# Kernel tuning notes

Hardware: AMD Instinct MI355X
Metric: run time of the kernel (lower is better)

Reference implementation:

```python
import jax, jax.numpy as jnp
import numpy as np

# dims: S=batch, P=num_patches, Q=patch_pixels, CB=convolution_bond, R=bond_dim, C=output classes, N=num_carriages
S, P, Q = 512, 196, 48
CB, R, C = 8, 32, 10
N = 8
SC = 0.05  # param init scale to keep the length-8 contraction chain numerically tame


def setup_inputs() -> dict:
    key = jax.random.key(0)
    ks = jax.random.split(key, 7)
    f32 = jnp.float32
    return {
        "x": jax.random.normal(ks[0], (S, P, Q), f32),
        # conv blocks: first has left CB bond squeezed, last has right CB bond squeezed
        "conv_first": jax.random.normal(ks[1], (Q, CB), f32) * SC,
        "conv_mid": jax.random.normal(ks[2], (N - 2, CB, Q, CB), f32) * SC,
        "conv_last": jax.random.normal(ks[3], (CB, Q), f32) * SC,
        # train blocks: first has r_l squeezed and carries the output index c;
        # middle/last have c=1 (squeezed); last has r_r squeezed
        "train_first": jax.random.normal(ks[4], (C, P, R), f32) * SC,
        "train_mid": jax.random.normal(ks[5], (N - 2, R, P, R), f32) * SC,
        "train_last": jax.random.normal(ks[6], (R, P), f32) * SC,
    }


def reference(x, conv_first, conv_mid, conv_last, train_first, train_mid, train_last):
    # Carriage 1: contract X with C1 over patch_pixels, with A1 over patches.
    # state[s, b(CB bond), r(train bond), c(output)]
    state = jnp.einsum('spq,qb,cpr->sbrc', x, conv_first, train_first)

    def step(state, blocks):
        Ck, Ak = blocks  # Ck: [a,q,b], Ak: [l,p,r]
        M = jnp.einsum('spq,aqb->spab', x, Ck)          # [s,p,a,b]
        G = jnp.einsum('spab,lpr->sablr', M, Ak)        # [s,a,b,l,r] per-carriage node
        # contract incoming CB bond (a) and train bond (l) with state
        new_state = jnp.einsum('salc,sablr->sbrc', state, G)
        return new_state, None

    state, _ = jax.lax.scan(step, state, (conv_mid, train_mid))

    # Last carriage: both right bonds squeezed
    GN = jnp.einsum('spq,aq,lp->sal', x, conv_last, train_last)  # [s,a,l]
    out = jnp.einsum('salc,sal->sc', state, GN)  # [S, C]
    return out
```

## Files before the change

### kernel.cpp

```cpp
#include <hip/hip_runtime.h>


typedef _Float16 half8 __attribute__((ext_vector_type(8)));
typedef _Float16 half4 __attribute__((ext_vector_type(4)));
typedef __fp16   fp16x2 __attribute__((ext_vector_type(2)));
typedef float floatx4 __attribute__((ext_vector_type(4)));

#define KP 224
#define LDA2 232
#define GSTR 40
#define SSTR 264

__device__ __forceinline__ void gld_lds16(const void* g, void* l) {
  __builtin_amdgcn_global_load_lds((const __attribute__((address_space(1))) void*)g,
                                   (__attribute__((address_space(3))) void*)l, 16, 0, 0);
}

__global__ __launch_bounds__(256)
void gemm_23(const _Float16* __restrict__ MtF, const _Float16* __restrict__ Bt0,
             const _Float16* __restrict__ MtL, const _Float16* __restrict__ Btl,
             float* __restrict__ stA, float* __restrict__ GN)
{
  __shared__ __align__(16) _Float16 Ash[128 * 32];
  __shared__ __align__(16) _Float16 Bsh[128 * 32];
  const int tid  = threadIdx.x;
  const int wave = tid >> 6;
  const int lane = tid & 63;
  const bool m2 = blockIdx.x < 3;
  const _Float16* A  = m2 ? MtF : MtL;
  const _Float16* Bt = m2 ? Bt0 : Btl;
  const int m0 = blockIdx.y * 128;
  const int n0 = m2 ? blockIdx.x * 128 : 0;
  const int wm = (wave >> 1) * 64;
  const int wn = (wave & 1) * 64;
  const int fr = lane & 15;
  const int fq = lane >> 4;

  floatx4 acc[4][4] = {};

  for (int kt = 0; kt < KP; kt += 32) {
    __syncthreads();
#pragma unroll
    for (int j = 0; j < 2; j++) {
      const int c   = j * 256 + tid;
      const int row = c >> 2;
      const int ko  = (c & 3) * 8;
      gld_lds16(A  + (size_t)(m0 + row) * KP + kt + ko,
                (char*)Ash + (size_t)(j * 256 + wave * 64) * 16);
      gld_lds16(Bt + (size_t)(n0 + row) * KP + kt + ko,
                (char*)Bsh + (size_t)(j * 256 + wave * 64) * 16);
    }
    __syncthreads();
    half8 af[4], bf[4];
#pragma unroll
    for (int i = 0; i < 4; i++)
      af[i] = *(const half8*)&Ash[(wm + i * 16 + fr) * 32 + fq * 8];
#pragma unroll
    for (int i = 0; i < 4; i++)
      bf[i] = *(const half8*)&Bsh[(wn + i * 16 + fr) * 32 + fq * 8];
#pragma unroll
    for (int i = 0; i < 4; i++)
#pragma unroll
      for (int j = 0; j < 4; j++)
        acc[i][j] = __builtin_amdgcn_mfma_f32_16x16x32_f16(af[i], bf[j], acc[i][j], 0, 0, 0);
  }

#pragma unroll
  for (int i = 0; i < 4; i++) {
#pragma unroll
    for (int j = 0; j < 4; j++) {
#pragma unroll
      for (int r = 0; r < 4; r++) {
        const int m = m0 + wm + i * 16 + fq * 4 + r;
        const int n = n0 + wn + j * 16 + fr;
        const float v = acc[i][j][r];
        if (m2) {
          if (n < 320) stA[(size_t)(m & 511) * 2560 + (m >> 9) * 320 + n] = v;
        } else {
          if (n < 32) GN[(size_t)m * 32 + n] = v;
        }
      }
    }
  }
}

__global__ __launch_bounds__(256)
void gemm_fl(const _Float16* __restrict__ xh2, const _Float16* __restrict__ Ckt,
             _Float16* __restrict__ MtF, _Float16* __restrict__ MtL)
{
  const int tid  = threadIdx.x;
  const int wave = tid >> 6;
  const int lane = tid & 63;
  const int fr = lane & 15;
  const int fq = lane >> 4;
  const int m0 = blockIdx.x * 128;

  const int crow = (fr < 8) ? fr : 384 + fr;
  const half8 b0 = *(const half8*)&Ckt[(size_t)crow * 64 + fq * 8];
  const half8 b1 = *(const half8*)&Ckt[(size_t)crow * 64 + 32 + fq * 8];

#pragma unroll
  for (int t = 0; t < 2; t++) {
    const int mi = wave * 2 + t;
    const int mrow = m0 + mi * 16 + fr;
    const half8 a0 = *(const half8*)&xh2[(size_t)mrow * 64 + fq * 8];
    const half8 a1 = *(const half8*)&xh2[(size_t)mrow * 64 + 32 + fq * 8];
    floatx4 c = {};
    c = __builtin_amdgcn_mfma_f32_16x16x32_f16(a0, b0, c, 0, 0, 0);
    c = __builtin_amdgcn_mfma_f32_16x16x32_f16(a1, b1, c, 0, 0, 0);
    const int m = m0 + mi * 16 + fq * 4;
    const unsigned s = (unsigned)m / 224u;
    const unsigned pp = (unsigned)m - s * 224u;
    half4 h;
#pragma unroll
    for (int r = 0; r < 4; r++) h[r] = (_Float16)c[r];
    if (fr < 8)
      *(half4*)&MtF[((size_t)fr * 512 + s) * KP + pp] = h;
    else
      *(half4*)&MtL[((size_t)(fr - 8) * 512 + s) * KP + pp] = h;
  }
}

__global__ __launch_bounds__(256, 2)
void chain_kernel(const _Float16* __restrict__ xh2, const _Float16* __restrict__ Ckt,
                  const _Float16* __restrict__ Akr, const float* __restrict__ St0,
                  const float* __restrict__ GN, float* __restrict__ out)
{
  __shared__ __align__(16) _Float16 Ash[64 * LDA2];
  __shared__ __align__(16) _Float16 Gsh[4][64 * GSTR];
  __shared__ __align__(16) _Float16 St3[16 * SSTR];
  __shared__ float oc[10];

  const int tid  = threadIdx.x;
  const int wave = tid >> 6;
  const int lane = tid & 63;
  const int s    = blockIdx.x;
  const int fr   = lane & 15;
  const int fq   = lane >> 4;
  const int fre  = fr & 7;
  const int frh  = fr >> 3;
  const int fqh  = fq >> 1;
  const int fql  = fq & 1;

  {
    const int b = tid >> 5, r = tid & 31;
    const int kcol = r * 8 + ((b & 1) * 4 + (b >> 1));
    const float* src = St0 + (size_t)s * 2560 + (size_t)tid * 10;
#pragma unroll
    for (int c = 0; c < 10; c++) St3[c * SSTR + kcol] = (_Float16)src[c];
    if (tid < 10) oc[tid] = 0.f;
  }

  const size_t lb0 = (size_t)((0 * 2 + frh) * 32 + wave * 8 + fre) * KP + fq * 8;
  const size_t lb1 = (size_t)((1 * 2 + frh) * 32 + wave * 8 + fre) * KP + fq * 8;

  half8 bq[2][2];
#pragma unroll
  for (int t2 = 0; t2 < 2; t2++) {
    bq[t2][0] = *(const half8*)(Akr + lb0 + t2 * 32);
    bq[t2][1] = *(const half8*)(Akr + lb1 + t2 * 32);
  }
  const _Float16* xb_base = xh2 + (size_t)s * 224 * 64;
  __syncthreads();

  _Float16* gw = &Gsh[wave][0];

  for (int k = 0; k < 6; k++) {
    {
      const _Float16* cb = Ckt + (size_t)(8 + k * 64 + wave * 16 + fr) * 64 + fq * 8;
      const half8 ca0 = *(const half8*)cb;
      const half8 ca1 = *(const half8*)(cb + 32);
      const _Float16* xr = xb_base + (size_t)fr * 64 + fq * 8;
      half8 xqA0 = *(const half8*)xr;
      half8 xqA1 = *(const half8*)(xr + 32);
      half8 xqB0 = *(const half8*)(xr + 16 * 64);
      half8 xqB1 = *(const half8*)(xr + 16 * 64 + 32);
      const int arow = (wave * 16 + fr) * LDA2 + fq * 4;
#pragma unroll 1
      for (int nt = 0; nt < 14; nt += 2) {
        floatx4 c0 = {};
        c0 = __builtin_amdgcn_mfma_f32_16x16x32_f16(xqA0, ca0, c0, 0, 0, 0);
        c0 = __builtin_amdgcn_mfma_f32_16x16x32_f16(xqA1, ca1, c0, 0, 0, 0);
        if (nt < 12) {
          const _Float16* xb = xr + (size_t)(nt + 2) * 16 * 64;
          xqA0 = *(const half8*)xb;
          xqA1 = *(const half8*)(xb + 32);
        }
        {
          half4 h;
#pragma unroll
          for (int r = 0; r < 4; r++) h[r] = (_Float16)c0[r];
          *(half4*)&Ash[arow + nt * 16] = h;
        }
        floatx4 c1 = {};
        c1 = __builtin_amdgcn_mfma_f32_16x16x32_f16(xqB0, ca0, c1, 0, 0, 0);
        c1 = __builtin_amdgcn_mfma_f32_16x16x32_f16(xqB1, ca1, c1, 0, 0, 0);
        if (nt < 12) {
          const _Float16* xb = xr + (size_t)(nt + 3) * 16 * 64;
          xqB0 = *(const half8*)xb;
          xqB1 = *(const half8*)(xb + 32);
        }
        {
          half4 h;
#pragma unroll
          for (int r = 0; r < 4; r++) h[r] = (_Float16)c1[r];
          *(half4*)&Ash[arow + (nt + 1) * 16] = h;
        }
      }
    }
    __syncthreads();

    half8 af[7][4];
#pragma unroll
    for (int kt = 0; kt < 7; kt++)
#pragma unroll
      for (int mi = 0; mi < 4; mi++)
        af[kt][mi] = *(const half8*)&Ash[(mi * 16 + fr) * LDA2 + kt * 32 + fq * 8];
    __syncthreads();

    floatx4 ns[4] = {};

#pragma unroll 1
    for (int cc = 0; cc < 8; cc++) {
      floatx4 acc[4][2] = {};
      const _Float16* Bc = Akr + ((size_t)k * 1024 + cc * 128) * KP;
#pragma unroll
      for (int kt = 0; kt < 7; kt++) {
#pragma unroll
        for (int mi = 0; mi < 4; mi++) {
          acc[mi][0] = __builtin_amdgcn_mfma_f32_16x16x32_f16(af[kt][mi], bq[kt & 1][0], acc[mi][0], 0, 0, 0);
          acc[mi][1] = __builtin_amdgcn_mfma_f32_16x16x32_f16(af[kt][mi], bq[kt & 1][1], acc[mi][1], 0, 0, 0);
        }
        if (kt < 5) {
          bq[kt & 1][0] = *(const half8*)(Bc + lb0 + (kt + 2) * 32);
          bq[kt & 1][1] = *(const half8*)(Bc + lb1 + (kt + 2) * 32);
        }
      }
      {
        int ncc = cc + 1, nk = k;
        if (ncc == 8) { ncc = 0; nk = k + 1; }
        if (nk < 6) {
          const _Float16* Bn = Akr + ((size_t)nk * 1024 + ncc * 128) * KP;
#pragma unroll
          for (int t2 = 0; t2 < 2; t2++) {
            bq[t2][0] = *(const half8*)(Bn + lb0 + t2 * 32);
            bq[t2][1] = *(const half8*)(Bn + lb1 + t2 * 32);
          }
        }
      }

#pragma unroll
      for (int ni = 0; ni < 2; ni++)
#pragma unroll
        for (int rg = 0; rg < 4; rg++) {
          union { half4 h4; fp16x2 p[2]; } u;
          u.p[0] = __builtin_amdgcn_cvt_pkrtz(acc[0][ni][rg], acc[1][ni][rg]);
          u.p[1] = __builtin_amdgcn_cvt_pkrtz(acc[2][ni][rg], acc[3][ni][rg]);
          *(half4*)&gw[((fql * 4 + rg) * 8 + fre) * GSTR + (ni * 2 + frh) * 8 + fqh * 4] = u.h4;
        }

      const half8 bs = *(const half8*)&St3[fr * SSTR + cc * 32 + fq * 8];
#pragma unroll
      for (int t = 0; t < 4; t++) {
        const half8 aa = *(const half8*)&gw[(t * 16 + fr) * GSTR + fq * 8];
        ns[t] = __builtin_amdgcn_mfma_f32_16x16x32_f16(aa, bs, ns[t], 0, 0, 0);
      }
    }

    __syncthreads();
    if (fr < 10) {
#pragma unroll
      for (int t = 0; t < 4; t++) {
#pragma unroll
        for (int rg = 0; rg < 4; rg++) {
          const int m = t * 16 + fq * 4 + rg;
          const int b = m >> 3, rr = m & 7;
          St3[fr * SSTR + (wave * 8 + rr) * 8 + (b & 1) * 4 + (b >> 1)] = (_Float16)ns[t][rg];
        }
      }
    }
  }
  __syncthreads();

  {
    const int a = tid >> 5, l = tid & 31;
    const float gn = GN[((size_t)a * 512 + s) * 32 + l];
    const int kcol = l * 8 + ((a & 1) * 4 + (a >> 1));
#pragma unroll
    for (int c = 0; c < 10; c++) {
      float v = gn * (float)St3[c * SSTR + kcol];
#pragma unroll
      for (int o2 = 1; o2 < 64; o2 <<= 1) v += __shfl_xor(v, o2, 64);
      if (lane == 0) atomicAdd(&oc[c], v);
    }
    __syncthreads();
    if (tid < 10) out[(size_t)s * 10 + tid] = oc[tid];
  }
}

__global__ void prep_all(const float* __restrict__ x, const float* __restrict__ cf,
                         const float* __restrict__ cm, const float* __restrict__ cl,
                         const float* __restrict__ tf, const float* __restrict__ tm,
                         const float* __restrict__ tl,
                         _Float16* __restrict__ xh2, _Float16* __restrict__ Ckt,
                         _Float16* __restrict__ Akr, _Float16* __restrict__ Bt0,
                         _Float16* __restrict__ Btl)
{
  const int bx = blockIdx.x;
  const int tid = threadIdx.x;
  if (bx < 3584) {
    const int i8 = bx * 256 + tid;
    const int q8 = (i8 & 7) * 8;
    const int spp = i8 >> 3;
    const unsigned s = (unsigned)spp / 224u;
    const unsigned pp = (unsigned)spp - s * 224u;
    half8 h = {};
    if (pp < 196 && q8 < 48) {
      const float* src = x + ((size_t)s * 196 + pp) * 48 + q8;
#pragma unroll
      for (int j = 0; j < 8; j++) h[j] = (_Float16)src[j];
    }
    *(half8*)&xh2[(size_t)spp * 64 + q8] = h;
  } else if (bx < 3712) {
    const int idx = (bx - 3584) * 256 + tid;
    const int q = idx & 63;
    const int row = idx >> 6;
    float v = 0.f;
    if (q < 48) {
      if (row < 8) v = cf[q * 8 + row];
      else if (row < 392) {
        const int rr = row - 8;
        const int k = rr >> 6, ab = rr & 63, a = ab >> 3, b = ab & 7;
        v = cm[((k * 8 + a) * 48 + q) * 8 + b];
      } else if (row < 400) v = cl[(row - 392) * 48 + q];
    }
    Ckt[idx] = (_Float16)v;
  } else if (bx < 9088) {
    const int idx = (bx - 3712) * 256 + tid;
    const int p = idx % 224;
    const int lr = (idx / 224) & 1023;
    const int k = idx / (224 * 1024);
    const int l = lr >> 5, r = lr & 31;
    float v = 0.f;
    if (p < 196) v = tm[(((k * 32 + l) * 196) + p) * 32 + r];
    Akr[idx] = (_Float16)v;
  } else if (bx < 9424) {
    const int idx = (bx - 9088) * 256 + tid;
    const int p = idx % 224;
    const int n = idx / 224;
    float v = 0.f;
    if (n < 320 && p < 196) {
      const int r = n / 10, c = n % 10;
      v = tf[(c * 196 + p) * 32 + r];
    }
    Bt0[idx] = (_Float16)v;
  } else {
    const int idx = (bx - 9424) * 256 + tid;
    const int p = idx % 224;
    const int n = idx / 224;
    float v = 0.f;
    if (n < 32 && p < 196) v = tl[n * 196 + p];
    Btl[idx] = (_Float16)v;
  }
}

extern "C" void kernel_launch(void* const* d_in, const int* in_sizes, int n_in,
                              void* d_out, int out_size, void* d_ws, size_t ws_size,
                              hipStream_t stream)
{
  const float* x  = (const float*)d_in[0];
  const float* cf = (const float*)d_in[1];
  const float* cm = (const float*)d_in[2];
  const float* cl = (const float*)d_in[3];
  const float* tf = (const float*)d_in[4];
  const float* tm = (const float*)d_in[5];
  const float* tl = (const float*)d_in[6];
  float* out = (float*)d_out;

  char* w = (char*)d_ws;
  auto alloc = [&](size_t bytes) { char* p = w; w += (bytes + 255) & ~(size_t)255; return p; };
  _Float16* xh2 = (_Float16*)alloc(512ull * 224 * 64 * 2);
  _Float16* Ckt = (_Float16*)alloc(512ull * 64 * 2);
  _Float16* MtF = (_Float16*)alloc(8ull * 512 * KP * 2);
  _Float16* MtL = (_Float16*)alloc(8ull * 512 * KP * 2);
  _Float16* Akr = (_Float16*)alloc(6ull * 1024 * KP * 2);
  _Float16* Bt0 = (_Float16*)alloc(384ull * KP * 2);
  _Float16* Btl = (_Float16*)alloc(128ull * KP * 2);
  float* stA    = (float*)alloc(512ull * 2560 * 4);
  float* GN     = (float*)alloc(4096ull * 32 * 4);
  (void)ws_size; (void)in_sizes; (void)n_in; (void)out_size;

  prep_all<<< 9536, 256, 0, stream>>>(x, cf, cm, cl, tf, tm, tl,
                                      xh2, Ckt, Akr, Bt0, Btl);
  gemm_fl <<<  896, 256, 0, stream>>>(xh2, Ckt, MtF, MtL);
  gemm_23 <<<dim3(4, 32), 256, 0, stream>>>(MtF, Bt0, MtL, Btl, stA, GN);
  chain_kernel<<<512, 256, 0, stream>>>(xh2, Ckt, Akr, stA, GN, out);
}
```

Before: 226.1 us.

## Fuse first and last carriage GEMMs into the per-sample chain kernel

Removes the separate gemm_fl and gemm_23 launches and computes each sample's first-carriage state and last-carriage GN vector inside chain_kernel. It uses MFMA on that sample's x rows and keeps the results in shared memory. This eliminates two kernel launches and the global round trips through MtF/MtL, stA and GN. The cost is extra per-block work and LDS use in chain_kernel, plus uncoalesced per-sample reads of Bt0/Btl, which may lengthen the chain kernel's critical path.

```diff
diff --git a/kernel.cpp b/kernel.cpp
--- a/kernel.cpp
+++ b/kernel.cpp
@@ -11,124 +11,15 @@
 #define GSTR 40
 #define SSTR 264
 
-__device__ __forceinline__ void gld_lds16(const void* g, void* l) {
-  __builtin_amdgcn_global_load_lds((const __attribute__((address_space(1))) void*)g,
-                                   (__attribute__((address_space(3))) void*)l, 16, 0, 0);
-}
-
-__global__ __launch_bounds__(256)
-void gemm_23(const _Float16* __restrict__ MtF, const _Float16* __restrict__ Bt0,
-             const _Float16* __restrict__ MtL, const _Float16* __restrict__ Btl,
-             float* __restrict__ stA, float* __restrict__ GN)
-{
-  __shared__ __align__(16) _Float16 Ash[128 * 32];
-  __shared__ __align__(16) _Float16 Bsh[128 * 32];
-  const int tid  = threadIdx.x;
-  const int wave = tid >> 6;
-  const int lane = tid & 63;
-  const bool m2 = blockIdx.x < 3;
-  const _Float16* A  = m2 ? MtF : MtL;
-  const _Float16* Bt = m2 ? Bt0 : Btl;
-  const int m0 = blockIdx.y * 128;
-  const int n0 = m2 ? blockIdx.x * 128 : 0;
-  const int wm = (wave >> 1) * 64;
-  const int wn = (wave & 1) * 64;
-  const int fr = lane & 15;
-  const int fq = lane >> 4;
-
-  floatx4 acc[4][4] = {};
-
-  for (int kt = 0; kt < KP; kt += 32) {
-    __syncthreads();
-#pragma unroll
-    for (int j = 0; j < 2; j++) {
-      const int c   = j * 256 + tid;
-      const int row = c >> 2;
-      const int ko  = (c & 3) * 8;
-      gld_lds16(A  + (size_t)(m0 + row) * KP + kt + ko,
-                (char*)Ash + (size_t)(j * 256 + wave * 64) * 16);
-      gld_lds16(Bt + (size_t)(n0 + row) * KP + kt + ko,
-                (char*)Bsh + (size_t)(j * 256 + wave * 64) * 16);
-    }
-    __syncthreads();
-    half8 af[4], bf[4];
-#pragma unroll
-    for (int i = 0; i < 4; i++)
-      af[i] = *(const half8*)&Ash[(wm + i * 16 + fr) * 32 + fq * 8];
-#pragma unroll
-    for (int i = 0; i < 4; i++)
-      bf[i] = *(const half8*)&Bsh[(wn + i * 16 + fr) * 32 + fq * 8];
-#pragma unroll
-    for (int i = 0; i < 4; i++)
-#pragma unroll
-      for (int j = 0; j < 4; j++)
-        acc[i][j] = __builtin_amdgcn_mfma_f32_16x16x32_f16(af[i], bf[j], acc[i][j], 0, 0, 0);
-  }
-
-#pragma unroll
-  for (int i = 0; i < 4; i++) {
-#pragma unroll
-    for (int j = 0; j < 4; j++) {
-#pragma unroll
-      for (int r = 0; r < 4; r++) {
-        const int m = m0 + wm + i * 16 + fq * 4 + r;
-        const int n = n0 + wn + j * 16 + fr;
-        const float v = acc[i][j][r];
-        if (m2) {
-          if (n < 320) stA[(size_t)(m & 511) * 2560 + (m >> 9) * 320 + n] = v;
-        } else {
-          if (n < 32) GN[(size_t)m * 32 + n] = v;
-        }
-      }
-    }
-  }
-}
-
-__global__ __launch_bounds__(256)
-void gemm_fl(const _Float16* __restrict__ xh2, const _Float16* __restrict__ Ckt,
-             _Float16* __restrict__ MtF, _Float16* __restrict__ MtL)
-{
-  const int tid  = threadIdx.x;
-  const int wave = tid >> 6;
-  const int lane = tid & 63;
-  const int fr = lane & 15;
-  const int fq = lane >> 4;
-  const int m0 = blockIdx.x * 128;
-
-  const int crow = (fr < 8) ? fr : 384 + fr;
-  const half8 b0 = *(const half8*)&Ckt[(size_t)crow * 64 + fq * 8];
-  const half8 b1 = *(const half8*)&Ckt[(size_t)crow * 64 + 32 + fq * 8];
-
-#pragma unroll
-  for (int t = 0; t < 2; t++) {
-    const int mi = wave * 2 + t;
-    const int mrow = m0 + mi * 16 + fr;
-    const half8 a0 = *(const half8*)&xh2[(size_t)mrow * 64 + fq * 8];
-    const half8 a1 = *(const half8*)&xh2[(size_t)mrow * 64 + 32 + fq * 8];
-    floatx4 c = {};
-    c = __builtin_amdgcn_mfma_f32_16x16x32_f16(a0, b0, c, 0, 0, 0);
-    c = __builtin_amdgcn_mfma_f32_16x16x32_f16(a1, b1, c, 0, 0, 0);
-    const int m = m0 + mi * 16 + fq * 4;
-    const unsigned s = (unsigned)m / 224u;
-    const unsigned pp = (unsigned)m - s * 224u;
-    half4 h;
-#pragma unroll
-    for (int r = 0; r < 4; r++) h[r] = (_Float16)c[r];
-    if (fr < 8)
-      *(half4*)&MtF[((size_t)fr * 512 + s) * KP + pp] = h;
-    else
-      *(half4*)&MtL[((size_t)(fr - 8) * 512 + s) * KP + pp] = h;
-  }
-}
-
 __global__ __launch_bounds__(256, 2)
 void chain_kernel(const _Float16* __restrict__ xh2, const _Float16* __restrict__ Ckt,
-                  const _Float16* __restrict__ Akr, const float* __restrict__ St0,
-                  const float* __restrict__ GN, float* __restrict__ out)
+                  const _Float16* __restrict__ Akr, const _Float16* __restrict__ Bt0,
+                  const _Float16* __restrict__ Btl, float* __restrict__ out)
 {
   __shared__ __align__(16) _Float16 Ash[64 * LDA2];
   __shared__ __align__(16) _Float16 Gsh[4][64 * GSTR];
   __shared__ __align__(16) _Float16 St3[16 * SSTR];
+  __shared__ float GNsh[8][32];
   __shared__ float oc[10];
 
   const int tid  = threadIdx.x;
@@ -142,14 +33,7 @@
   const int fqh  = fq >> 1;
   const int fql  = fq & 1;
 
-  {
-    const int b = tid >> 5, r = tid & 31;
-    const int kcol = r * 8 + ((b & 1) * 4 + (b >> 1));
-    const float* src = St0 + (size_t)s * 2560 + (size_t)tid * 10;
-#pragma unroll
-    for (int c = 0; c < 10; c++) St3[c * SSTR + kcol] = (_Float16)src[c];
-    if (tid < 10) oc[tid] = 0.f;
-  }
+  if (tid < 10) oc[tid] = 0.f;
 
   const size_t lb0 = (size_t)((0 * 2 + frh) * 32 + wave * 8 + fre) * KP + fq * 8;
   const size_t lb1 = (size_t)((1 * 2 + frh) * 32 + wave * 8 + fre) * KP + fq * 8;
@@ -161,7 +45,71 @@
     bq[t2][1] = *(const half8*)(Akr + lb1 + t2 * 32);
   }
   const _Float16* xb_base = xh2 + (size_t)s * 224 * 64;
+
+  _Float16* Fsh = &Gsh[0][0];
+
+  {
+    const int crow = (fr < 8) ? fr : 384 + fr;
+    const half8 ca0 = *(const half8*)&Ckt[(size_t)crow * 64 + fq * 8];
+    const half8 ca1 = *(const half8*)&Ckt[(size_t)crow * 64 + 32 + fq * 8];
+#pragma unroll
+    for (int j = 0; j < 4; j++) {
+      const int nt = wave + j * 4;
+      if (nt < 14) {
+        const _Float16* xb = xb_base + (size_t)(nt * 16 + fr) * 64 + fq * 8;
+        const half8 xb0 = *(const half8*)xb;
+        const half8 xb1 = *(const half8*)(xb + 32);
+        floatx4 c = {};
+        c = __builtin_amdgcn_mfma_f32_16x16x32_f16(ca0, xb0, c, 0, 0, 0);
+        c = __builtin_amdgcn_mfma_f32_16x16x32_f16(ca1, xb1, c, 0, 0, 0);
+#pragma unroll
+        for (int r = 0; r < 4; r++)
+          Fsh[(fq * 4 + r) * LDA2 + nt * 16 + fr] = (_Float16)c[r];
+      }
+    }
+  }
   __syncthreads();
+
+  {
+    floatx4 pc[5] = {};
+#pragma unroll 1
+    for (int kt = 0; kt < 7; kt++) {
+      const half8 fa = *(const half8*)&Fsh[fr * LDA2 + kt * 32 + fq * 8];
+#pragma unroll
+      for (int j = 0; j < 5; j++) {
+        const int rcrow = (wave * 5 + j) * 16 + fr;
+        const half8 bb = *(const half8*)&Bt0[(size_t)rcrow * KP + kt * 32 + fq * 8];
+        pc[j] = __builtin_amdgcn_mfma_f32_16x16x32_f16(fa, bb, pc[j], 0, 0, 0);
+      }
+    }
+    if (fq < 2) {
+#pragma unroll
+      for (int j = 0; j < 5; j++) {
+        const int rc = (wave * 5 + j) * 16 + fr;
+        const int r10 = (int)(((unsigned)rc * 205u) >> 11);
+        const int c = rc - r10 * 10;
+#pragma unroll
+        for (int ri = 0; ri < 4; ri++) {
+          const int b = fq * 4 + ri;
+          St3[c * SSTR + r10 * 8 + ((b & 1) * 4 + (b >> 1))] = (_Float16)pc[j][ri];
+        }
+      }
+    }
+  }
+  if (wave < 2) {
+    floatx4 gc = {};
+#pragma unroll 1
+    for (int kt = 0; kt < 7; kt++) {
+      const half8 fa = *(const half8*)&Fsh[fr * LDA2 + kt * 32 + fq * 8];
+      const half8 bb = *(const half8*)&Btl[(size_t)(wave * 16 + fr) * KP + kt * 32 + fq * 8];
+      gc = __builtin_amdgcn_mfma_f32_16x16x32_f16(fa, bb, gc, 0, 0, 0);
+    }
+    if (fq >= 2) {
+#pragma unroll
+      for (int ri = 0; ri < 4; ri++)
+        GNsh[(fq - 2) * 4 + ri][wave * 16 + fr] = gc[ri];
+    }
+  }
 
   _Float16* gw = &Gsh[wave][0];
 
@@ -284,7 +232,7 @@
 
   {
     const int a = tid >> 5, l = tid & 31;
-    const float gn = GN[((size_t)a * 512 + s) * 32 + l];
+    const float gn = GNsh[a][l];
     const int kcol = l * 8 + ((a & 1) * 4 + (a >> 1));
 #pragma unroll
     for (int c = 0; c < 10; c++) {
@@ -381,18 +329,12 @@
   auto alloc = [&](size_t bytes) { char* p = w; w += (bytes + 255) & ~(size_t)255; return p; };
   _Float16* xh2 = (_Float16*)alloc(512ull * 224 * 64 * 2);
   _Float16* Ckt = (_Float16*)alloc(512ull * 64 * 2);
-  _Float16* MtF = (_Float16*)alloc(8ull * 512 * KP * 2);
-  _Float16* MtL = (_Float16*)alloc(8ull * 512 * KP * 2);
   _Float16* Akr = (_Float16*)alloc(6ull * 1024 * KP * 2);
   _Float16* Bt0 = (_Float16*)alloc(384ull * KP * 2);
   _Float16* Btl = (_Float16*)alloc(128ull * KP * 2);
-  float* stA    = (float*)alloc(512ull * 2560 * 4);
-  float* GN     = (float*)alloc(4096ull * 32 * 4);
   (void)ws_size; (void)in_sizes; (void)n_in; (void)out_size;
 
   prep_all<<< 9536, 256, 0, stream>>>(x, cf, cm, cl, tf, tm, tl,
                                       xh2, Ckt, Akr, Bt0, Btl);
-  gemm_fl <<<  896, 256, 0, stream>>>(xh2, Ckt, MtF, MtL);
-  gemm_23 <<<dim3(4, 32), 256, 0, stream>>>(MtF, Bt0, MtL, Btl, stA, GN);
-  chain_kernel<<<512, 256, 0, stream>>>(xh2, Ckt, Akr, stA, GN, out);
+  chain_kernel<<<512, 256, 0, stream>>>(xh2, Ckt, Akr, Bt0, Btl, out);
 }
```

Measured after the change: 220.4 us. -2.5%, faster.
